# Performance work log

Hardware: AMD Instinct MI355X
Metric: run time of the kernel (lower is better)

The kernel has to match this reference:

```python
import jax, jax.numpy as jnp
import numpy as np

N = 50000   # num_entities
E = 600000  # num_edges
D = 128     # dim
R = 200     # num_relations
T = 1000    # num_timestamps
L = 2       # num_layers


def setup_inputs() -> dict:
    key = jax.random.key(0)
    ks = jax.random.split(key, 16)
    edge_index = jax.random.randint(ks[0], (2, E), 0, N)
    edge_type = jax.random.randint(ks[1], (E,), 0, R)
    edge_time = jax.random.randint(ks[2], (E,), 0, T)
    edge_weight = jax.random.uniform(ks[3], (E,), dtype=jnp.float32)
    perm = jax.random.permutation(ks[4], N)
    entity_emb = jax.random.normal(ks[5], (N, D), dtype=jnp.float32)
    rel_emb = jax.random.normal(ks[6], (R, D), dtype=jnp.float32)
    time_emb = jax.random.normal(ks[7], (T, D), dtype=jnp.float32)
    s = 1.0 / np.sqrt(D)
    in_proj_w = jax.random.uniform(ks[8], (L, D, 2 * D), minval=-s, maxval=s)
    in_proj_b = jax.random.uniform(ks[9], (L, 2 * D), minval=-s, maxval=s)
    out_proj_w = jax.random.uniform(ks[10], (L, D, D), minval=-s, maxval=s)
    out_proj_b = jax.random.uniform(ks[11], (L, D), minval=-s, maxval=s)
    A = jax.random.normal(ks[12], (L, D)) * 0.1
    B = jax.random.normal(ks[13], (L, D)) * 0.1
    ln_g = jnp.ones((L, D), dtype=jnp.float32)
    ln_b = jnp.zeros((L, D), dtype=jnp.float32)
    return dict(edge_index=edge_index, edge_type=edge_type, edge_time=edge_time,
                edge_weight=edge_weight, perm=perm, entity_emb=entity_emb,
                rel_emb=rel_emb, time_emb=time_emb, in_proj_w=in_proj_w,
                in_proj_b=in_proj_b, out_proj_w=out_proj_w, out_proj_b=out_proj_b,
                A=A, B=B, ln_g=ln_g, ln_b=ln_b)


def _mamba_layer(x, Wi, bi, Wo, bo, A, B, g_ln, b_ln):
    # x: [N, D]
    zg = x @ Wi + bi                      # [N, 2D]
    z, g = jnp.split(zg, 2, axis=-1)
    g = jax.nn.sigmoid(g)

    def step(prev, zg_i):
        z_i, g_i = zg_i
        curr = g_i * (A * prev) + B * z_i
        return curr, curr

    _, h = jax.lax.scan(step, jnp.zeros((D,), x.dtype), (z, g))  # [N, D]
    y = x + h @ Wo + bo
    mu = jnp.mean(y, axis=-1, keepdims=True)
    var = jnp.mean((y - mu) ** 2, axis=-1, keepdims=True)
    return (y - mu) / jnp.sqrt(var + 1e-5) * g_ln + b_ln


def reference(edge_index, edge_type, edge_time, edge_weight, perm, entity_emb,
              rel_emb, time_emb, in_proj_w, in_proj_b, out_proj_w, out_proj_b,
              A, B, ln_g, ln_b):
    src, dst = edge_index[0], edge_index[1]
    msgs = entity_emb[src] + rel_emb[edge_type] + time_emb[edge_time]  # [E, D]
    sums = jax.ops.segment_sum(msgs * edge_weight[:, None], dst, num_segments=N)
    cnt = jax.ops.segment_sum(edge_weight, dst, num_segments=N)
    x = sums / jnp.maximum(cnt, 1.0)[:, None]          # scatter_mean
    x = x / jnp.maximum(jnp.linalg.norm(x, axis=1, keepdims=True), 1e-12)
    x = x[perm]
    for l in range(L):
        x = _mamba_layer(x, in_proj_w[l], in_proj_b[l], out_proj_w[l],
                         out_proj_b[l], A[l], B[l], ln_g[l], ln_b[l])
    return x
```

## Files before the change

### kernel.cpp

```cpp
#include <hip/hip_runtime.h>
#include <hip/hip_bf16.h>

typedef unsigned short ushort_t;
typedef unsigned int   uint_t;
typedef __attribute__((ext_vector_type(8))) short bf8;
typedef __attribute__((ext_vector_type(4))) float f32x4;

constexpr int N = 50000;
constexpr int E = 600000;
constexpr int D = 128;
constexpr int L = 2;
constexpr int NB = (N + 255) / 256;

constexpr int TR   = 64;
constexpr int LOOK = 16;
constexpr int RT   = TR + LOOK;
constexpr int NBLK = (N + TR - 1) / TR;

constexpr int SM_ZS  = 0;
constexpr int SM_GS  = 20992;
constexpr int SM_HS  = 41984;
constexpr int SM_RED = 59392;
constexpr int SM_TOT = 59904;

__device__ __forceinline__ float us2f(ushort_t u) {
    union { uint_t i; float f; } c; c.i = (uint_t)u << 16; return c.f;
}
__device__ __forceinline__ ushort_t f2us(float f) {
    __hip_bfloat16 b = __float2bfloat16(f);
    return *(ushort_t*)&b;
}

__global__ __launch_bounds__(256) void k_hist(
    const int* __restrict__ dstp, int* __restrict__ hist)
{
    int e = blockIdx.x * 256 + threadIdx.x;
    if (e < E) atomicAdd(&hist[dstp[e]], 1);
}

__global__ __launch_bounds__(256) void k_scan1(
    const int* __restrict__ hist, int* __restrict__ part, int* __restrict__ bsum)
{
    int i = blockIdx.x * 256 + threadIdx.x;
    int v = (i < N) ? hist[i] : 0;
    int lane = threadIdx.x & 63, wv = threadIdx.x >> 6;
    int s = v;
    #pragma unroll
    for (int m = 1; m < 64; m <<= 1) {
        int t = __shfl_up(s, m, 64);
        if (lane >= m) s += t;
    }
    __shared__ int wsum[4];
    if (lane == 63) wsum[wv] = s;
    __syncthreads();
    int off = 0;
    for (int w = 0; w < wv; w++) off += wsum[w];
    if (i < N) part[i] = s - v + off;
    if (threadIdx.x == 255)
        bsum[blockIdx.x] = wsum[0] + wsum[1] + wsum[2] + wsum[3];
}

__global__ __launch_bounds__(256) void k_scan2(int* __restrict__ bsum)
{
    int i = threadIdx.x;
    int v = (i < NB) ? bsum[i] : 0;
    int lane = i & 63, wv = i >> 6;
    int s = v;
    #pragma unroll
    for (int m = 1; m < 64; m <<= 1) {
        int t = __shfl_up(s, m, 64);
        if (lane >= m) s += t;
    }
    __shared__ int wsum[4];
    if (lane == 63) wsum[wv] = s;
    __syncthreads();
    int off = 0;
    for (int w = 0; w < wv; w++) off += wsum[w];
    if (i < NB) bsum[i] = s - v + off;
}

__global__ __launch_bounds__(256) void k_finalize(
    const int* __restrict__ part, const int* __restrict__ bsum,
    int* __restrict__ cursor, int* __restrict__ rowst,
    const int* __restrict__ perm, int* __restrict__ invp)
{
    int i = blockIdx.x * 256 + threadIdx.x;
    if (i < N) {
        int b = part[i] + bsum[i >> 8];
        cursor[i] = b;
        rowst[i] = b;
        invp[perm[i]] = i;
    }
}

__global__ __launch_bounds__(256) void k_scatter(
    const int* __restrict__ eidx, const int* __restrict__ etype,
    const int* __restrict__ etime, const float* __restrict__ ew,
    int* __restrict__ cursor, int2* __restrict__ esort)
{
    int e = blockIdx.x * 256 + threadIdx.x;
    if (e >= E) return;
    int dst = eidx[E + e];
    int slot = atomicAdd(&cursor[dst], 1);
    int2 p;
    p.x = (eidx[e] & 0xffff) | (etype[e] << 16);
    p.y = (etime[e] & 0xffff) | ((int)f2us(ew[e]) << 16);
    esort[slot] = p;
}

__global__ __launch_bounds__(256) void k_ctab(
    const float* __restrict__ ent, const float* __restrict__ rel,
    const float* __restrict__ tim, ushort_t* __restrict__ entb,
    ushort_t* __restrict__ relb, ushort_t* __restrict__ timb)
{
    size_t t = (size_t)blockIdx.x * 256 + threadIdx.x;
    const float2* s; uint_t* d; size_t off;
    if (t < 3200000)        { s = (const float2*)ent; d = (uint_t*)entb; off = t; }
    else if (t < 3212800)   { s = (const float2*)rel; d = (uint_t*)relb; off = t - 3200000; }
    else if (t < 3276800)   { s = (const float2*)tim; d = (uint_t*)timb; off = t - 3212800; }
    else return;
    float2 v = s[off];
    d[off] = (uint_t)f2us(v.x) | ((uint_t)f2us(v.y) << 16);
}

__global__ __launch_bounds__(256) void k_castw(
    const float* __restrict__ Wi, const float* __restrict__ Wo,
    ushort_t* __restrict__ WiT, ushort_t* __restrict__ WoT)
{
    int t = blockIdx.x * 256 + threadIdx.x;
    if (t < L * 256 * 128) {
        int l = t / (256 * 128), r = t % (256 * 128);
        int n = r / 128, k = r % 128;
        WiT[t] = f2us(Wi[(size_t)l * 128 * 256 + k * 256 + n]);
    } else if (t < L * 256 * 128 + L * 128 * 128) {
        int u = t - L * 256 * 128;
        int l = u / (128 * 128), r = u % (128 * 128);
        int n = r / 128, k = r % 128;
        WoT[u] = f2us(Wo[(size_t)l * 128 * 128 + k * 128 + n]);
    }
}

__global__ __launch_bounds__(256) void k_agg(
    const int2* __restrict__ esort, const int* __restrict__ rowst,
    const int* __restrict__ hist, const int* __restrict__ invp,
    const ushort_t* __restrict__ entb, const ushort_t* __restrict__ relb,
    const ushort_t* __restrict__ timb, ushort_t* __restrict__ xbf)
{
    int wv = threadIdx.x >> 6, lane = threadIdx.x & 63;
    int d = blockIdx.x * 4 + wv;
    if (d >= N) return;
    int beg = rowst[d];
    int n = hist[d];

    float a0 = 0.f, a1 = 0.f, b0 = 0.f, b1 = 0.f, ws0 = 0.f, ws1 = 0.f;
    int j = 0;
    for (; j + 1 < n; j += 2) {
        int2 p = esort[beg + j];
        int2 q = esort[beg + j + 1];
        int  ps = p.x & 0xffff, pt = ((uint_t)p.x) >> 16;
        int  qs = q.x & 0xffff, qt = ((uint_t)q.x) >> 16;
        int  pm = p.y & 0xffff, qm = q.y & 0xffff;
        float wp = us2f((ushort_t)(((uint_t)p.y) >> 16));
        float wq = us2f((ushort_t)(((uint_t)q.y) >> 16));
        uint_t pa = *(const uint_t*)(entb + (size_t)ps * D + 2 * lane);
        uint_t qa = *(const uint_t*)(entb + (size_t)qs * D + 2 * lane);
        uint_t pb = *(const uint_t*)(relb + (size_t)pt * D + 2 * lane);
        uint_t qb = *(const uint_t*)(relb + (size_t)qt * D + 2 * lane);
        uint_t pc = *(const uint_t*)(timb + (size_t)pm * D + 2 * lane);
        uint_t qc = *(const uint_t*)(timb + (size_t)qm * D + 2 * lane);
        a0 += (us2f(pa & 0xffff) + us2f(pb & 0xffff) + us2f(pc & 0xffff)) * wp;
        a1 += (us2f(pa >> 16)    + us2f(pb >> 16)    + us2f(pc >> 16))    * wp;
        b0 += (us2f(qa & 0xffff) + us2f(qb & 0xffff) + us2f(qc & 0xffff)) * wq;
        b1 += (us2f(qa >> 16)    + us2f(qb >> 16)    + us2f(qc >> 16))    * wq;
        ws0 += wp; ws1 += wq;
    }
    if (j < n) {
        int2 p = esort[beg + j];
        int  ps = p.x & 0xffff, pt = ((uint_t)p.x) >> 16;
        int  pm = p.y & 0xffff;
        float wp = us2f((ushort_t)(((uint_t)p.y) >> 16));
        uint_t pa = *(const uint_t*)(entb + (size_t)ps * D + 2 * lane);
        uint_t pb = *(const uint_t*)(relb + (size_t)pt * D + 2 * lane);
        uint_t pc = *(const uint_t*)(timb + (size_t)pm * D + 2 * lane);
        a0 += (us2f(pa & 0xffff) + us2f(pb & 0xffff) + us2f(pc & 0xffff)) * wp;
        a1 += (us2f(pa >> 16)    + us2f(pb >> 16)    + us2f(pc >> 16))    * wp;
        ws0 += wp;
    }
    a0 += b0; a1 += b1;
    float inv = 1.0f / fmaxf(ws0 + ws1, 1.0f);
    a0 *= inv; a1 *= inv;

    float ss = a0 * a0 + a1 * a1;
    #pragma unroll
    for (int m = 32; m >= 1; m >>= 1) ss += __shfl_xor(ss, m, 64);
    float sc = 1.0f / fmaxf(sqrtf(ss), 1e-12f);

    int orow = invp[d];
    uint_t out = (uint_t)f2us(a0 * sc) | ((uint_t)f2us(a1 * sc) << 16);
    *(uint_t*)(xbf + (size_t)orow * D + 2 * lane) = out;
}

template <bool FINAL>
__global__ __launch_bounds__(256, 2) void k_layer(
    const ushort_t* __restrict__ xin, const ushort_t* __restrict__ WiT,
    const float* __restrict__ bi, const ushort_t* __restrict__ WoT,
    const float* __restrict__ bo, const float* __restrict__ Aw,
    const float* __restrict__ Bw, const float* __restrict__ lg,
    const float* __restrict__ lb, ushort_t* __restrict__ xoutb,
    float* __restrict__ outf)
{
    __shared__ char sm[SM_TOT];
    ushort_t* zs  = (ushort_t*)(sm + SM_ZS);
    ushort_t* gs  = (ushort_t*)(sm + SM_GS);
    ushort_t* hs  = (ushort_t*)(sm + SM_HS);
    float*    red = (float*)(sm + SM_RED);
    float*    ys  = (float*)sm;

    int tid = threadIdx.x;
    int w = tid >> 6, lane = tid & 63;
    int quad = lane >> 4, m = lane & 15;
    int r0 = blockIdx.x * TR;
    int base = r0 - LOOK;

    const bf8 zero8 = {0, 0, 0, 0, 0, 0, 0, 0};
    const f32x4 zero4 = {0.f, 0.f, 0.f, 0.f};

    {
        int cb = w * 64;
        bf8 bfrag[4][4];
        #pragma unroll
        for (int sub = 0; sub < 4; sub++)
            #pragma unroll
            for (int kb = 0; kb < 4; kb++)
                bfrag[sub][kb] = *(const bf8*)(WiT + (size_t)(cb + sub * 16 + m) * 128
                                               + kb * 32 + quad * 8);
        #pragma unroll
        for (int rt = 0; rt < 5; rt++) {
            int gr = base + rt * 16 + m;
            bf8 a[4];
            if (gr >= 0 && gr < N) {
                #pragma unroll
                for (int kb = 0; kb < 4; kb++)
                    a[kb] = *(const bf8*)(xin + (size_t)gr * 128 + kb * 32 + quad * 8);
            } else {
                #pragma unroll
                for (int kb = 0; kb < 4; kb++) a[kb] = zero8;
            }
            f32x4 acc[4] = {zero4, zero4, zero4, zero4};
            #pragma unroll
            for (int sub = 0; sub < 4; sub++)
                #pragma unroll
                for (int kb = 0; kb < 4; kb++)
                    acc[sub] = __builtin_amdgcn_mfma_f32_16x16x32_bf16(
                        a[kb], bfrag[sub][kb], acc[sub], 0, 0, 0);
            #pragma unroll
            for (int sub = 0; sub < 4; sub++) {
                int col = cb + sub * 16 + m;
                float bias = bi[col];
                #pragma unroll
                for (int reg = 0; reg < 4; reg++) {
                    int rr = rt * 16 + quad * 4 + reg;
                    float v = acc[sub][reg] + bias;
                    if (col < 128)
                        zs[col * 82 + rr] = f2us(v);
                    else
                        gs[(col - 128) * 82 + rr] = f2us(1.f / (1.f + __expf(-v)));
                }
            }
        }
    }
    __syncthreads();

    if (tid < 128) {
        int dd = tid;
        float Ad = Aw[dd], Bd = Bw[dd], h = 0.f;
        int rrs = (base < 0) ? LOOK : 0;
        int lim = N - base; if (lim > RT) lim = RT;
        for (int rr = rrs; rr < lim; ++rr) {
            float z = us2f(zs[dd * 82 + rr]);
            float g = us2f(gs[dd * 82 + rr]);
            h = g * (Ad * h) + Bd * z;
            if (rr >= LOOK) hs[(rr - LOOK) * 136 + dd] = f2us(h);
        }
    }
    __syncthreads();

    {
        int cb = w * 32;
        bf8 b2[2][4];
        #pragma unroll
        for (int sub = 0; sub < 2; sub++)
            #pragma unroll
            for (int kb = 0; kb < 4; kb++)
                b2[sub][kb] = *(const bf8*)(WoT + (size_t)(cb + sub * 16 + m) * 128
                                            + kb * 32 + quad * 8);
        #pragma unroll
        for (int rt = 0; rt < 4; rt++) {
            bf8 a[4];
            #pragma unroll
            for (int kb = 0; kb < 4; kb++)
                a[kb] = *(const bf8*)(hs + (rt * 16 + m) * 136 + kb * 32 + quad * 8);
            f32x4 acc[2] = {zero4, zero4};
            #pragma unroll
            for (int sub = 0; sub < 2; sub++)
                #pragma unroll
                for (int kb = 0; kb < 4; kb++)
                    acc[sub] = __builtin_amdgcn_mfma_f32_16x16x32_bf16(
                        a[kb], b2[sub][kb], acc[sub], 0, 0, 0);
            #pragma unroll
            for (int sub = 0; sub < 2; sub++) {
                int col = cb + sub * 16 + m;
                float bias = bo[col];
                #pragma unroll
                for (int reg = 0; reg < 4; reg++) {
                    int rr = rt * 16 + quad * 4 + reg;
                    int gr = r0 + rr;
                    float res = (gr < N) ? us2f(xin[(size_t)gr * 128 + col]) : 0.f;
                    ys[rr * 132 + col] = acc[sub][reg] + bias + res;
                }
            }
        }
    }
    __syncthreads();

    {
        int row = tid >> 2, part = tid & 3;
        float s = 0.f, ss = 0.f;
        #pragma unroll
        for (int i = 0; i < 32; i++) {
            float v = ys[row * 132 + part * 32 + i];
            s += v; ss += v * v;
        }
        s += __shfl_xor(s, 1, 64); ss += __shfl_xor(ss, 1, 64);
        s += __shfl_xor(s, 2, 64); ss += __shfl_xor(ss, 2, 64);
        if (part == 0) {
            float mu = s * (1.f / 128.f);
            float var = ss * (1.f / 128.f) - mu * mu;
            red[row] = mu;
            red[64 + row] = rsqrtf(var + 1e-5f);
        }
    }
    __syncthreads();

    #pragma unroll
    for (int i = 0; i < 32; i++) {
        int flat = i * 256 + tid;
        int rr = flat >> 7, col = flat & 127;
        int gr = r0 + rr;
        if (gr < N) {
            float v = (ys[rr * 132 + col] - red[rr]) * red[64 + rr] * lg[col] + lb[col];
            if (FINAL) outf[(size_t)gr * 128 + col] = v;
            else       xoutb[(size_t)gr * 128 + col] = f2us(v);
        }
    }
}

extern "C" void kernel_launch(void* const* d_in, const int* in_sizes, int n_in,
                              void* d_out, int out_size, void* d_ws, size_t ws_size,
                              hipStream_t stream)
{
    const int*   eidx  = (const int*)d_in[0];
    const int*   etype = (const int*)d_in[1];
    const int*   etime = (const int*)d_in[2];
    const float* ew    = (const float*)d_in[3];
    const int*   perm  = (const int*)d_in[4];
    const float* ent   = (const float*)d_in[5];
    const float* rel   = (const float*)d_in[6];
    const float* tim   = (const float*)d_in[7];
    const float* Wi    = (const float*)d_in[8];
    const float* bi    = (const float*)d_in[9];
    const float* Wo    = (const float*)d_in[10];
    const float* bo    = (const float*)d_in[11];
    const float* Aw    = (const float*)d_in[12];
    const float* Bw    = (const float*)d_in[13];
    const float* lg    = (const float*)d_in[14];
    const float* lbp   = (const float*)d_in[15];

    char* base = (char*)d_ws;
    size_t o = 0;
    ushort_t* xbf  = (ushort_t*)(base + o); o += (size_t)N * D * 2;
    ushort_t* xb2  = (ushort_t*)(base + o); o += (size_t)N * D * 2;
    ushort_t* entb = (ushort_t*)(base + o); o += (size_t)N * D * 2;
    ushort_t* relb = (ushort_t*)(base + o); o += (size_t)200 * D * 2;
    ushort_t* timb = (ushort_t*)(base + o); o += (size_t)1000 * D * 2;
    ushort_t* WiT  = (ushort_t*)(base + o); o += (size_t)L * 256 * 128 * 2;
    ushort_t* WoT  = (ushort_t*)(base + o); o += (size_t)L * 128 * 128 * 2;
    int2*     esort  = (int2*)(base + o);   o += (size_t)E * 8;
    int*      hist   = (int*)(base + o);    o += (size_t)N * 4;
    int*      part   = (int*)(base + o);    o += (size_t)N * 4;
    int*      bsum   = (int*)(base + o);    o += 256 * 4;
    int*      cursor = (int*)(base + o);    o += (size_t)N * 4;
    int*      rowst  = (int*)(base + o);    o += (size_t)N * 4;
    int*      invp   = (int*)(base + o);    o += (size_t)N * 4;

    hipMemsetAsync(hist, 0, N * sizeof(int), stream);

    k_ctab    <<<12800, 256, 0, stream>>>(ent, rel, tim, entb, relb, timb);
    k_castw   <<<(L * 256 * 128 + L * 128 * 128 + 255) / 256, 256, 0, stream>>>(
                Wi, Wo, WiT, WoT);
    k_hist    <<<(E + 255) / 256, 256, 0, stream>>>(eidx + E, hist);
    k_scan1   <<<NB, 256, 0, stream>>>(hist, part, bsum);
    k_scan2   <<<1, 256, 0, stream>>>(bsum);
    k_finalize<<<NB, 256, 0, stream>>>(part, bsum, cursor, rowst, perm, invp);
    k_scatter <<<(E + 255) / 256, 256, 0, stream>>>(eidx, etype, etime, ew,
                                                    cursor, esort);
    k_agg     <<<(N + 3) / 4, 256, 0, stream>>>(esort, rowst, hist, invp,
                                                entb, relb, timb, xbf);

    k_layer<false><<<NBLK, 256, 0, stream>>>(
        xbf, WiT, bi, WoT, bo, Aw, Bw, lg, lbp, xb2, nullptr);
    k_layer<true><<<NBLK, 256, 0, stream>>>(
        xb2, WiT + (size_t)256 * 128, bi + 256, WoT + (size_t)128 * 128,
        bo + 128, Aw + 128, Bw + 128, lg + 128, lbp + 128,
        nullptr, (float*)d_out);
}
```

Measured before the change: 345.4 us.

## Shrink layer tile and shared memory, keep outputs in registers for layernorm

Shrinks the layer tile from 64 to 48 rows and interleaves z and g into a single packed shared array that also holds h in place, cutting LDS use so four blocks per CU can run instead of two. The out-projection results stay in registers, and layernorm statistics are computed with wave shuffles plus a small cross-wave reduction instead of staging y in shared memory. The scan gets an unrolled fast path for interior blocks. In exchange, the fixed 16-row lookahead costs a larger share of work per block, and the h tile is read back with strided scalar LDS loads.

```diff
diff --git a/kernel.cpp b/kernel.cpp
--- a/kernel.cpp
+++ b/kernel.cpp
@@ -12,16 +12,11 @@
 constexpr int L = 2;
 constexpr int NB = (N + 255) / 256;
 
-constexpr int TR   = 64;
+constexpr int TR   = 48;
 constexpr int LOOK = 16;
 constexpr int RT   = TR + LOOK;
 constexpr int NBLK = (N + TR - 1) / TR;
-
-constexpr int SM_ZS  = 0;
-constexpr int SM_GS  = 20992;
-constexpr int SM_HS  = 41984;
-constexpr int SM_RED = 59392;
-constexpr int SM_TOT = 59904;
+constexpr int SD   = 67;
 
 __device__ __forceinline__ float us2f(ushort_t u) {
     union { uint_t i; float f; } c; c.i = (uint_t)u << 16; return c.f;
@@ -201,7 +196,7 @@
 }
 
 template <bool FINAL>
-__global__ __launch_bounds__(256, 2) void k_layer(
+__global__ __launch_bounds__(256, 4) void k_layer(
     const ushort_t* __restrict__ xin, const ushort_t* __restrict__ WiT,
     const float* __restrict__ bi, const ushort_t* __restrict__ WoT,
     const float* __restrict__ bo, const float* __restrict__ Aw,
@@ -209,12 +204,12 @@
     const float* __restrict__ lb, ushort_t* __restrict__ xoutb,
     float* __restrict__ outf)
 {
-    __shared__ char sm[SM_TOT];
-    ushort_t* zs  = (ushort_t*)(sm + SM_ZS);
-    ushort_t* gs  = (ushort_t*)(sm + SM_GS);
-    ushort_t* hs  = (ushort_t*)(sm + SM_HS);
-    float*    red = (float*)(sm + SM_RED);
-    float*    ys  = (float*)sm;
+    __shared__ uint_t zgp[128 * SD];
+    ushort_t* zg16 = (ushort_t*)zgp;
+    float*    redS = (float*)zgp;
+    float*    redQ = redS + 192;
+    float*    muA  = redS + 384;
+    float*    rsA  = redS + 432;
 
     int tid = threadIdx.x;
     int w = tid >> 6, lane = tid & 63;
@@ -227,44 +222,48 @@
 
     {
         int cb = w * 64;
-        bf8 bfrag[4][4];
         #pragma unroll
-        for (int sub = 0; sub < 4; sub++)
-            #pragma unroll
-            for (int kb = 0; kb < 4; kb++)
-                bfrag[sub][kb] = *(const bf8*)(WiT + (size_t)(cb + sub * 16 + m) * 128
-                                               + kb * 32 + quad * 8);
-        #pragma unroll
-        for (int rt = 0; rt < 5; rt++) {
-            int gr = base + rt * 16 + m;
-            bf8 a[4];
-            if (gr >= 0 && gr < N) {
-                #pragma unroll
-                for (int kb = 0; kb < 4; kb++)
-                    a[kb] = *(const bf8*)(xin + (size_t)gr * 128 + kb * 32 + quad * 8);
-            } else {
-                #pragma unroll
-                for (int kb = 0; kb < 4; kb++) a[kb] = zero8;
-            }
-            f32x4 acc[4] = {zero4, zero4, zero4, zero4};
-            #pragma unroll
-            for (int sub = 0; sub < 4; sub++)
-                #pragma unroll
-                for (int kb = 0; kb < 4; kb++)
-                    acc[sub] = __builtin_amdgcn_mfma_f32_16x16x32_bf16(
-                        a[kb], bfrag[sub][kb], acc[sub], 0, 0, 0);
-            #pragma unroll
-            for (int sub = 0; sub < 4; sub++) {
-                int col = cb + sub * 16 + m;
-                float bias = bi[col];
+        for (int sp = 0; sp < 2; sp++) {
+            int c0 = cb + sp * 32 + m, c1 = c0 + 16;
+            float bias0 = bi[c0], bias1 = bi[c1];
+            bf8 b0[4], b1[4];
+            #pragma unroll
+            for (int kb = 0; kb < 4; kb++) {
+                b0[kb] = *(const bf8*)(WiT + (size_t)c0 * 128 + kb * 32 + quad * 8);
+                b1[kb] = *(const bf8*)(WiT + (size_t)c1 * 128 + kb * 32 + quad * 8);
+            }
+            #pragma unroll
+            for (int rt = 0; rt < 4; rt++) {
+                int gr = base + rt * 16 + m;
+                bf8 a[4];
+                if (gr >= 0 && gr < N) {
+                    #pragma unroll
+                    for (int kb = 0; kb < 4; kb++)
+                        a[kb] = *(const bf8*)(xin + (size_t)gr * 128 + kb * 32 + quad * 8);
+                } else {
+                    #pragma unroll
+                    for (int kb = 0; kb < 4; kb++) a[kb] = zero8;
+                }
+                f32x4 acc0 = zero4, acc1 = zero4;
+                #pragma unroll
+                for (int kb = 0; kb < 4; kb++) {
+                    acc0 = __builtin_amdgcn_mfma_f32_16x16x32_bf16(a[kb], b0[kb], acc0, 0, 0, 0);
+                    acc1 = __builtin_amdgcn_mfma_f32_16x16x32_bf16(a[kb], b1[kb], acc1, 0, 0, 0);
+                }
                 #pragma unroll
                 for (int reg = 0; reg < 4; reg++) {
                     int rr = rt * 16 + quad * 4 + reg;
-                    float v = acc[sub][reg] + bias;
-                    if (col < 128)
-                        zs[col * 82 + rr] = f2us(v);
-                    else
-                        gs[(col - 128) * 82 + rr] = f2us(1.f / (1.f + __expf(-v)));
+                    float v0 = acc0[reg] + bias0;
+                    float v1 = acc1[reg] + bias1;
+                    if (c0 < 128) {
+                        zg16[(c0 * SD + rr) * 2] = f2us(v0);
+                        zg16[(c1 * SD + rr) * 2] = f2us(v1);
+                    } else {
+                        zg16[((c0 - 128) * SD + rr) * 2 + 1] =
+                            f2us(1.f / (1.f + __expf(-v0)));
+                        zg16[((c1 - 128) * SD + rr) * 2 + 1] =
+                            f2us(1.f / (1.f + __expf(-v1)));
+                    }
                 }
             }
         }
@@ -272,86 +271,140 @@
     __syncthreads();
 
     if (tid < 128) {
-        int dd = tid;
-        float Ad = Aw[dd], Bd = Bw[dd], h = 0.f;
-        int rrs = (base < 0) ? LOOK : 0;
-        int lim = N - base; if (lim > RT) lim = RT;
-        for (int rr = rrs; rr < lim; ++rr) {
-            float z = us2f(zs[dd * 82 + rr]);
-            float g = us2f(gs[dd * 82 + rr]);
-            h = g * (Ad * h) + Bd * z;
-            if (rr >= LOOK) hs[(rr - LOOK) * 136 + dd] = f2us(h);
+        int d = tid;
+        const uint_t* col = zgp + d * SD;
+        ushort_t* hcol = (ushort_t*)col;
+        float Ad = Aw[d], Bd = Bw[d], h = 0.f;
+        if (base >= 0 && base + RT <= N) {
+            #pragma unroll
+            for (int b8 = 0; b8 < 8; b8++) {
+                uint_t v[8];
+                #pragma unroll
+                for (int k = 0; k < 8; k++) v[k] = col[b8 * 8 + k];
+                #pragma unroll
+                for (int k = 0; k < 8; k++) {
+                    int rr = b8 * 8 + k;
+                    float z = us2f((ushort_t)(v[k] & 0xffff));
+                    float g = us2f((ushort_t)(v[k] >> 16));
+                    h = g * (Ad * h) + Bd * z;
+                    if (rr >= LOOK) hcol[rr * 2] = f2us(h);
+                }
+            }
+        } else {
+            int s = (base < 0) ? LOOK : 0;
+            int lim = N - base; if (lim > RT) lim = RT;
+            for (int rr = s; rr < lim; rr++) {
+                uint_t v = col[rr];
+                float z = us2f((ushort_t)(v & 0xffff));
+                float g = us2f((ushort_t)(v >> 16));
+                h = g * (Ad * h) + Bd * z;
+                if (rr >= LOOK) hcol[rr * 2] = f2us(h);
+            }
         }
     }
     __syncthreads();
 
+    float y[3][2][4];
     {
         int cb = w * 32;
-        bf8 b2[2][4];
+        int c0 = cb + m, c1 = c0 + 16;
+        float bias0 = bo[c0], bias1 = bo[c1];
+        bf8 b0[4], b1[4];
         #pragma unroll
-        for (int sub = 0; sub < 2; sub++)
-            #pragma unroll
-            for (int kb = 0; kb < 4; kb++)
-                b2[sub][kb] = *(const bf8*)(WoT + (size_t)(cb + sub * 16 + m) * 128
-                                            + kb * 32 + quad * 8);
+        for (int kb = 0; kb < 4; kb++) {
+            b0[kb] = *(const bf8*)(WoT + (size_t)c0 * 128 + kb * 32 + quad * 8);
+            b1[kb] = *(const bf8*)(WoT + (size_t)c1 * 128 + kb * 32 + quad * 8);
+        }
         #pragma unroll
-        for (int rt = 0; rt < 4; rt++) {
+        for (int rt = 0; rt < 3; rt++) {
+            int hrow = rt * 16 + m + LOOK;
             bf8 a[4];
             #pragma unroll
-            for (int kb = 0; kb < 4; kb++)
-                a[kb] = *(const bf8*)(hs + (rt * 16 + m) * 136 + kb * 32 + quad * 8);
-            f32x4 acc[2] = {zero4, zero4};
-            #pragma unroll
-            for (int sub = 0; sub < 2; sub++)
-                #pragma unroll
-                for (int kb = 0; kb < 4; kb++)
-                    acc[sub] = __builtin_amdgcn_mfma_f32_16x16x32_bf16(
-                        a[kb], b2[sub][kb], acc[sub], 0, 0, 0);
-            #pragma unroll
-            for (int sub = 0; sub < 2; sub++) {
-                int col = cb + sub * 16 + m;
-                float bias = bo[col];
+            for (int kb = 0; kb < 4; kb++) {
+                #pragma unroll
+                for (int j = 0; j < 8; j++)
+                    a[kb][j] = (short)zg16[((kb * 32 + quad * 8 + j) * SD + hrow) * 2];
+            }
+            f32x4 acc0 = zero4, acc1 = zero4;
+            #pragma unroll
+            for (int kb = 0; kb < 4; kb++) {
+                acc0 = __builtin_amdgcn_mfma_f32_16x16x32_bf16(a[kb], b0[kb], acc0, 0, 0, 0);
+                acc1 = __builtin_amdgcn_mfma_f32_16x16x32_bf16(a[kb], b1[kb], acc1, 0, 0, 0);
+            }
+            #pragma unroll
+            for (int reg = 0; reg < 4; reg++) {
+                int gr = r0 + rt * 16 + quad * 4 + reg;
+                float r0v = 0.f, r1v = 0.f;
+                if (gr < N) {
+                    r0v = us2f(xin[(size_t)gr * 128 + c0]);
+                    r1v = us2f(xin[(size_t)gr * 128 + c1]);
+                }
+                y[rt][0][reg] = acc0[reg] + bias0 + r0v;
+                y[rt][1][reg] = acc1[reg] + bias1 + r1v;
+            }
+        }
+    }
+    __syncthreads();
+
+    {
+        float ps[3][4], pq[3][4];
+        #pragma unroll
+        for (int rt = 0; rt < 3; rt++)
+            #pragma unroll
+            for (int reg = 0; reg < 4; reg++) {
+                float v0 = y[rt][0][reg], v1 = y[rt][1][reg];
+                float s = v0 + v1, q = v0 * v0 + v1 * v1;
+                #pragma unroll
+                for (int mk = 1; mk <= 8; mk <<= 1) {
+                    s += __shfl_xor(s, mk, 64);
+                    q += __shfl_xor(q, mk, 64);
+                }
+                ps[rt][reg] = s; pq[rt][reg] = q;
+            }
+        if (m == 0) {
+            #pragma unroll
+            for (int rt = 0; rt < 3; rt++)
                 #pragma unroll
                 for (int reg = 0; reg < 4; reg++) {
-                    int rr = rt * 16 + quad * 4 + reg;
-                    int gr = r0 + rr;
-                    float res = (gr < N) ? us2f(xin[(size_t)gr * 128 + col]) : 0.f;
-                    ys[rr * 132 + col] = acc[sub][reg] + bias + res;
-                }
-            }
+                    int row = rt * 16 + quad * 4 + reg;
+                    redS[row * 4 + w] = ps[rt][reg];
+                    redQ[row * 4 + w] = pq[rt][reg];
+                }
         }
     }
     __syncthreads();
-
+    if (tid < 48) {
+        float s = redS[tid * 4] + redS[tid * 4 + 1] + redS[tid * 4 + 2] + redS[tid * 4 + 3];
+        float q = redQ[tid * 4] + redQ[tid * 4 + 1] + redQ[tid * 4 + 2] + redQ[tid * 4 + 3];
+        float mu = s * (1.f / 128.f);
+        float var = q * (1.f / 128.f) - mu * mu;
+        muA[tid] = mu;
+        rsA[tid] = rsqrtf(var + 1e-5f);
+    }
+    __syncthreads();
     {
-        int row = tid >> 2, part = tid & 3;
-        float s = 0.f, ss = 0.f;
+        int cb = w * 32;
+        int c0 = cb + m, c1 = c0 + 16;
+        float gl0 = lg[c0], gl1 = lg[c1], bl0 = lb[c0], bl1 = lb[c1];
         #pragma unroll
-        for (int i = 0; i < 32; i++) {
-            float v = ys[row * 132 + part * 32 + i];
-            s += v; ss += v * v;
-        }
-        s += __shfl_xor(s, 1, 64); ss += __shfl_xor(ss, 1, 64);
-        s += __shfl_xor(s, 2, 64); ss += __shfl_xor(ss, 2, 64);
-        if (part == 0) {
-            float mu = s * (1.f / 128.f);
-            float var = ss * (1.f / 128.f) - mu * mu;
-            red[row] = mu;
-            red[64 + row] = rsqrtf(var + 1e-5f);
-        }
-    }
-    __syncthreads();
-
-    #pragma unroll
-    for (int i = 0; i < 32; i++) {
-        int flat = i * 256 + tid;
-        int rr = flat >> 7, col = flat & 127;
-        int gr = r0 + rr;
-        if (gr < N) {
-            float v = (ys[rr * 132 + col] - red[rr]) * red[64 + rr] * lg[col] + lb[col];
-            if (FINAL) outf[(size_t)gr * 128 + col] = v;
-            else       xoutb[(size_t)gr * 128 + col] = f2us(v);
-        }
+        for (int rt = 0; rt < 3; rt++)
+            #pragma unroll
+            for (int reg = 0; reg < 4; reg++) {
+                int rr = rt * 16 + quad * 4 + reg;
+                int gr = r0 + rr;
+                if (gr < N) {
+                    float mu = muA[rr], rs = rsA[rr];
+                    float v0 = (y[rt][0][reg] - mu) * rs * gl0 + bl0;
+                    float v1 = (y[rt][1][reg] - mu) * rs * gl1 + bl1;
+                    if (FINAL) {
+                        outf[(size_t)gr * 128 + c0] = v0;
+                        outf[(size_t)gr * 128 + c1] = v1;
+                    } else {
+                        xoutb[(size_t)gr * 128 + c0] = f2us(v0);
+                        xoutb[(size_t)gr * 128 + c1] = f2us(v1);
+                    }
+                }
+            }
     }
 }
 
```

After: 330.4 us. 1.05x faster.
